# Performance work log

Hardware: AMD Instinct MI355X
Metric: run time of the kernel (lower is better)

The kernel has to match this reference:

```python
import jax, jax.numpy as jnp
import numpy as np

B = 16384; NF = 16; VOCAB = 100000; ED = 32; NNUM = 13
E = 8; T = 2; H0 = 512; H1 = 256; TH = 128
D0 = NF * ED + NNUM  # 525
EPS = 1e-5


def setup_inputs() -> dict:
    key = jax.random.key(0)
    ks = jax.random.split(key, 24)
    f32 = jnp.float32
    return {
        "categorical_x": jax.random.randint(ks[0], (B, NF), 0, VOCAB),
        "numerical_x": jax.random.normal(ks[1], (B, NNUM), f32),
        "epoch": 5,  # >= M -> MoE (not if_neuron) branch
        "emb_table": jax.random.normal(ks[2], (NF * VOCAB, ED), f32) * 0.05,
        "W0": jax.random.normal(ks[3], (E, D0, H0), f32) * 0.05,
        "b0": jnp.zeros((E, H0), f32),
        "bn0_gamma": 1.0 + 0.1 * jax.random.normal(ks[4], (H0,), f32),
        "bn0_beta": 0.1 * jax.random.normal(ks[5], (H0,), f32),
        "bn0_mean": 0.1 * jax.random.normal(ks[6], (H0,), f32),
        "bn0_var": 0.5 + jax.random.uniform(ks[7], (H0,), f32),
        "W1": jax.random.normal(ks[8], (E, H0, H1), f32) * 0.05,
        "b1": jnp.zeros((E, H1), f32),
        "bn1_gamma": 1.0 + 0.1 * jax.random.normal(ks[9], (H1,), f32),
        "bn1_beta": 0.1 * jax.random.normal(ks[10], (H1,), f32),
        "bn1_mean": 0.1 * jax.random.normal(ks[11], (H1,), f32),
        "bn1_var": 0.5 + jax.random.uniform(ks[12], (H1,), f32),
        "Wg": jax.random.normal(ks[13], (T, D0, E), f32) * 0.05,
        "bg": jnp.zeros((T, E), f32),
        "Wt1": jax.random.normal(ks[14], (T, H1, TH), f32) * 0.05,
        "bt1": jnp.zeros((T, TH), f32),
        "tbn_gamma": 1.0 + 0.1 * jax.random.normal(ks[15], (T, TH), f32),
        "tbn_beta": 0.1 * jax.random.normal(ks[16], (T, TH), f32),
        "tbn_mean": 0.1 * jax.random.normal(ks[17], (T, TH), f32),
        "tbn_var": 0.5 + jax.random.uniform(ks[18], (T, TH), f32),
        "Wt2": jax.random.normal(ks[19], (T, TH, 1), f32) * 0.05,
        "bt2": jnp.zeros((T, 1), f32),
    }


def reference(categorical_x, numerical_x, epoch, emb_table,
              W0, b0, bn0_gamma, bn0_beta, bn0_mean, bn0_var,
              W1, b1, bn1_gamma, bn1_beta, bn1_mean, bn1_var,
              Wg, bg, Wt1, bt1, tbn_gamma, tbn_beta, tbn_mean, tbn_var,
              Wt2, bt2):
    # --- embedding + concat ---
    offsets = jnp.arange(NF, dtype=categorical_x.dtype) * VOCAB
    emb = emb_table[categorical_x + offsets[None, :]].reshape(B, NF * ED)
    x = jnp.concatenate([emb, numerical_x], axis=1)  # [B, D0]

    def bn(h, g, b, m, v):  # eval-mode BatchNorm1d, params shared across experts
        return (h - m) * jax.lax.rsqrt(v + EPS) * g + b

    # --- per-expert layer 0: grouped GEMM + shared BN/ReLU (Dropout eval=id) ---
    h = jnp.einsum('bd,edk->ebk', x, W0) + b0[:, None, :]          # [E,B,H0]
    h = jax.nn.relu(bn(h, bn0_gamma, bn0_beta, bn0_mean, bn0_var))
    # --- per-expert layer 1 ---
    h = jnp.einsum('ebd,edk->ebk', h, W1) + b1[:, None, :]          # [E,B,H1]
    h = jax.nn.relu(bn(h, bn1_gamma, bn1_beta, bn1_mean, bn1_var))

    expert_output = jnp.transpose(h, (1, 0, 2))                     # [B,E,H1]
    # --- per-task softmax gates over the raw input, bmm combine ---
    gates = jax.nn.softmax(jnp.einsum('bd,tde->tbe', x, Wg) + bg[:, None, :], axis=-1)  # [T,B,E]
    fea = jnp.einsum('tbe,bek->tbk', gates, expert_output)          # [T,B,H1]

    # --- per-task tower MLP: Linear -> BN -> ReLU -> Linear, sigmoid ---
    t = jnp.einsum('tbk,tkh->tbh', fea, Wt1) + bt1[:, None, :]      # [T,B,TH]
    t = (t - tbn_mean[:, None, :]) * jax.lax.rsqrt(tbn_var[:, None, :] + EPS)
    t = jax.nn.relu(t * tbn_gamma[:, None, :] + tbn_beta[:, None, :])
    out = (jnp.einsum('tbh,tho->tbo', t, Wt2) + bt2[:, None, :])[..., 0]  # [T,B]
    return jax.nn.sigmoid(out)
```

## Files before the change

### kernel.cpp

```cpp
#include <hip/hip_runtime.h>
#include <hip/hip_bf16.h>

#define B_ 16384
#define NF_ 16
#define VOCAB_ 100000
#define ED_ 32
#define NNUM_ 13
#define E_ 8
#define T_ 2
#define H0_ 512
#define H1_ 256
#define TH_ 128
#define D0_ 525
#define K0P 640

typedef __bf16 bf16x8 __attribute__((ext_vector_type(8)));
typedef float  f32x4  __attribute__((ext_vector_type(4)));

typedef __attribute__((address_space(3))) void lds_void;
typedef __attribute__((address_space(1))) const void gbl_void;

__device__ __forceinline__ void load_lds16f(const void* g, void* l) {
  __builtin_amdgcn_global_load_lds((gbl_void*)g, (lds_void*)l, 16, 0, 0);
}

#define BARX                                        \
  do {                                              \
    asm volatile("" ::: "memory");                  \
    __builtin_amdgcn_s_barrier();                   \
    __builtin_amdgcn_sched_barrier(0);              \
    asm volatile("" ::: "memory");                  \
  } while (0)
#define LGKM0                                       \
  do {                                              \
    asm volatile("s_waitcnt lgkmcnt(0)" ::: "memory"); \
    __builtin_amdgcn_sched_barrier(0);              \
  } while (0)

__global__ __launch_bounds__(256) void k_embed(const int* __restrict__ cat,
                                               const float* __restrict__ num,
                                               const float* __restrict__ emb,
                                               __hip_bfloat16* __restrict__ x) {
  int b = blockIdx.x;
  int t = threadIdx.x;
  const int* crow = cat + b * NF_;
#pragma unroll
  for (int i = 0; i < 3; ++i) {
    int d = t + i * 256;
    if (d >= K0P) continue;
    float v;
    if (d < 512) {
      int f = d >> 5, c = d & 31;
      v = emb[((long long)(f * VOCAB_ + crow[f])) * ED_ + c];
    } else if (d < D0_) {
      v = num[b * NNUM_ + (d - 512)];
    } else {
      v = 0.f;
    }
    x[(long long)b * K0P + d] = __float2bfloat16(v);
  }
}

__global__ __launch_bounds__(256) void k_wprep(const float* __restrict__ W,
                                               __hip_bfloat16* __restrict__ Wp,
                                               int K, int N, int KP) {
  __shared__ float tile[64][65];
  int k0 = blockIdx.x * 64, n0 = blockIdx.y * 64, e = blockIdx.z;
  int tx = threadIdx.x & 63, ty = threadIdx.x >> 6;
  for (int r = ty; r < 64; r += 4) {
    int k = k0 + r;
    tile[r][tx] = (k < K) ? W[((long long)e * K + k) * N + n0 + tx] : 0.f;
  }
  __syncthreads();
  for (int r = ty; r < 64; r += 4) {
    int n = n0 + r;
    Wp[((long long)e * N + n) * KP + k0 + tx] = __float2bfloat16(tile[tx][r]);
  }
}

__global__ void k_prep_small(const float* b0, const float* g0, const float* be0,
                             const float* m0, const float* v0,
                             const float* b1, const float* g1, const float* be1,
                             const float* m1, const float* v1,
                             const float* bt1, const float* tg, const float* tb,
                             const float* tm, const float* tv,
                             float* scale0, float* ebias0, float* scale1, float* ebias1,
                             float* tscale, float* tbias) {
  int i = blockIdx.x * 256 + threadIdx.x;
  if (i < H0_) scale0[i] = g0[i] * rsqrtf(v0[i] + 1e-5f);
  if (i < H1_) scale1[i] = g1[i] * rsqrtf(v1[i] + 1e-5f);
  if (i < T_ * TH_) {
    float s = tg[i] * rsqrtf(tv[i] + 1e-5f);
    tscale[i] = s;
    tbias[i] = (bt1[i] - tm[i]) * s + tb[i];
  }
  if (i < E_ * H0_) {
    int n = i & (H0_ - 1);
    float s = g0[n] * rsqrtf(v0[n] + 1e-5f);
    ebias0[i] = (b0[i] - m0[n]) * s + be0[n];
  }
  if (i < E_ * H1_) {
    int n = i & (H1_ - 1);
    float s = g1[n] * rsqrtf(v1[n] + 1e-5f);
    ebias1[i] = (b1[i] - m1[n]) * s + be1[n];
  }
}

__global__ __launch_bounds__(256) void k_gates(const __hip_bfloat16* __restrict__ x,
                                               const float* __restrict__ Wg,
                                               const float* __restrict__ bg,
                                               float* __restrict__ gates) {
  int gidx = blockIdx.x * 256 + threadIdx.x;
  int b = gidx >> 4, te = gidx & 15;
  int t = te >> 3, e = te & 7;
  const __hip_bfloat16* xr = x + (long long)b * K0P;
  const float* wg = Wg + ((long long)t * D0_) * E_ + e;
  float acc = bg[t * E_ + e];
  int k = 0;
  for (; k + 8 <= D0_; k += 8) {
    bf16x8 xv = *reinterpret_cast<const bf16x8*>(xr + k);
#pragma unroll
    for (int j = 0; j < 8; ++j)
      acc += (float)xv[j] * wg[(long long)(k + j) * E_];
  }
  for (; k < D0_; ++k) acc += __bfloat162float(xr[k]) * wg[(long long)k * E_];
  float mx = acc;
#pragma unroll
  for (int o = 1; o < 8; o <<= 1) mx = fmaxf(mx, __shfl_xor(mx, o));
  float p = __expf(acc - mx);
  float s = p;
#pragma unroll
  for (int o = 1; o < 8; o <<= 1) s += __shfl_xor(s, o);
  gates[((long long)t * B_ + b) * E_ + e] = p / s;
}

__global__ __launch_bounds__(512, 2) void k_gemm(
    const __hip_bfloat16* __restrict__ Aall, long long strideAe, int lda,
    const __hip_bfloat16* __restrict__ Ball, long long strideBe, int ldb,
    __hip_bfloat16* __restrict__ Call, long long strideCe, int N,
    const float* __restrict__ scale, const float* __restrict__ ebias, int strideEb,
    int K) {
  __shared__ __align__(16) char As[2][2][16384];
  __shared__ __align__(16) char Bs[2][2][16384];

  const int e = blockIdx.z;
  const char* A = reinterpret_cast<const char*>(Aall + (long long)e * strideAe +
                                                (long long)blockIdx.x * 256 * lda);
  const char* Bw = reinterpret_cast<const char*>(Ball + (long long)e * strideBe +
                                                 (long long)blockIdx.y * 256 * ldb);
  const int ldab = lda * 2, ldbb = ldb * 2;

  const int tid = threadIdx.x;
  const int lane = tid & 63;
  const int wid = tid >> 6;
  const int wq_r = wid >> 2, wq_c = wid & 3;

  const int srow = tid >> 3;
  const int swz = ((tid & 7) << 4) ^ ((srow & 7) << 4);

  auto STG_A = [&](int kt, int half, int slot) {
#pragma unroll
    for (int j = 0; j < 2; ++j) {
      const int lrow = srow + j * 64;
      load_lds16f(A + (long long)(half * 128 + lrow) * ldab + kt * 128 + swz,
                  &As[slot][half][j * 8192 + tid * 16]);
    }
  };
  auto STG_B = [&](int kt, int half, int slot) {
#pragma unroll
    for (int j = 0; j < 2; ++j) {
      const int lrow = srow + j * 64;
      load_lds16f(Bw + (long long)(half * 128 + lrow) * ldbb + kt * 128 + swz,
                  &Bs[slot][half][j * 8192 + tid * 16]);
    }
  };

  bf16x8 af[2][4], bq[2][2];
  auto LDA = [&](int slot, int half) {
#pragma unroll
    for (int kk = 0; kk < 2; ++kk) {
      const int kb = kk * 64 + (lane >> 4) * 16;
#pragma unroll
      for (int m = 0; m < 4; ++m) {
        const int lrow = wq_r * 64 + m * 16 + (lane & 15);
        af[kk][m] = *reinterpret_cast<const bf16x8*>(
            &As[slot][half][lrow * 128 + (kb ^ ((lane & 7) << 4))]);
      }
    }
  };
  auto LDB = [&](int slot, int half) {
#pragma unroll
    for (int kk = 0; kk < 2; ++kk) {
      const int kb = kk * 64 + (lane >> 4) * 16;
#pragma unroll
      for (int n = 0; n < 2; ++n) {
        const int lrow = wq_c * 32 + n * 16 + (lane & 15);
        bq[kk][n] = *reinterpret_cast<const bf16x8*>(
            &Bs[slot][half][lrow * 128 + (kb ^ ((lane & 7) << 4))]);
      }
    }
  };

  f32x4 acc[2][2][4][2];
#pragma unroll
  for (int a = 0; a < 2; ++a)
#pragma unroll
    for (int b = 0; b < 2; ++b)
#pragma unroll
      for (int m = 0; m < 4; ++m)
#pragma unroll
        for (int n = 0; n < 2; ++n) acc[a][b][m][n] = (f32x4){0.f, 0.f, 0.f, 0.f};

#define MMQ(QM, QN)                                                            \
  do {                                                                         \
    __builtin_amdgcn_s_setprio(1);                                             \
    _Pragma("unroll") for (int kk = 0; kk < 2; ++kk)                           \
        _Pragma("unroll") for (int m = 0; m < 4; ++m)                          \
            _Pragma("unroll") for (int n = 0; n < 2; ++n)                      \
                acc[QM][QN][m][n] = __builtin_amdgcn_mfma_f32_16x16x32_bf16(   \
                    af[kk][m], bq[kk][n], acc[QM][QN][m][n], 0, 0, 0);         \
    __builtin_amdgcn_s_setprio(0);                                             \
  } while (0)

  const int nk = K / 64;
  const int nj = nk / 2;

  STG_A(0, 0, 0); STG_A(0, 1, 0); STG_B(0, 0, 0); STG_B(0, 1, 0);
  if (nk > 1) { STG_A(1, 0, 1); STG_B(1, 1, 1); }
  asm volatile("s_waitcnt vmcnt(4)" ::: "memory");
  BARX;

  for (int j = 0; j < nj; ++j) {
    const int t1 = 2 * j + 1, t2 = 2 * j + 2, t3 = 2 * j + 3;
    const bool more = (t2 < nk);
    LDA(0, 0); LDB(0, 0);
    STG_A(t1, 1, 1);
    BARX; LGKM0; MMQ(0, 0); BARX;
    LDB(0, 1);
    STG_B(t1, 0, 1);
    BARX; LGKM0; MMQ(0, 1); BARX;
    LDA(0, 1);
    if (more) STG_A(t2, 0, 0);
    BARX; LGKM0; MMQ(1, 1); BARX;
    LDB(0, 0);
    if (more) STG_B(t2, 1, 0);
    BARX; LGKM0; MMQ(1, 0);
    if (more) { asm volatile("s_waitcnt vmcnt(4)" ::: "memory"); }
    else      { asm volatile("s_waitcnt vmcnt(0)" ::: "memory"); }
    BARX;
    LDA(1, 0); LDB(1, 0);
    if (more) STG_A(t2, 1, 0);
    BARX; LGKM0; MMQ(0, 0); BARX;
    LDB(1, 1);
    if (more) STG_B(t2, 0, 0);
    BARX; LGKM0; MMQ(0, 1); BARX;
    LDA(1, 1);
    if (more) STG_A(t3, 0, 1);
    BARX; LGKM0; MMQ(1, 1); BARX;
    LDB(1, 0);
    if (more) STG_B(t3, 1, 1);
    BARX; LGKM0; MMQ(1, 0);
    if (more) { asm volatile("s_waitcnt vmcnt(4)" ::: "memory"); }
    BARX;
  }
#undef MMQ

  __hip_bfloat16* C = Call + (long long)e * strideCe;
  const float* eb = ebias + e * strideEb;
  const int m0 = blockIdx.x * 256, n0 = blockIdx.y * 256;
#pragma unroll
  for (int Qm = 0; Qm < 2; ++Qm)
#pragma unroll
    for (int Qn = 0; Qn < 2; ++Qn)
#pragma unroll
      for (int n = 0; n < 2; ++n) {
        const int col = n0 + Qn * 128 + wq_c * 32 + n * 16 + (lane & 15);
        const float s = scale[col];
        const float bb = eb[col];
#pragma unroll
        for (int m = 0; m < 4; ++m) {
          const int rowb = m0 + Qm * 128 + wq_r * 64 + m * 16 + (lane >> 4) * 4;
#pragma unroll
          for (int i = 0; i < 4; ++i) {
            float v = fmaxf(acc[Qm][Qn][m][n][i] * s + bb, 0.f);
            C[(long long)(rowb + i) * N + col] = __float2bfloat16(v);
          }
        }
      }
}

__global__ __launch_bounds__(256) void k_tower(
    const __hip_bfloat16* __restrict__ h1, const float* __restrict__ gates,
    const float* __restrict__ Wt1, const float* __restrict__ Wt2,
    const float* __restrict__ bt2, const float* __restrict__ tscale,
    const float* __restrict__ tbias, float* __restrict__ out) {
  __shared__ __align__(16) char Ws[TH_ * 512];
  const int tid = threadIdx.x;
  const int lane = tid & 63, wv = tid >> 6;

  const int row = blockIdx.x * 64 + wv * 16 + (lane & 15);
  const int g4 = lane >> 4;

  float gt0[8], gt1[8];
  {
    const float* gp0 = gates + (long long)row * E_;
    const float* gp1 = gates + ((long long)B_ + row) * E_;
#pragma unroll
    for (int j = 0; j < 8; ++j) { gt0[j] = gp0[j]; gt1[j] = gp1[j]; }
  }

  float fa0[8][8], fa1[8][8];
#pragma unroll
  for (int c = 0; c < 8; ++c)
#pragma unroll
    for (int j = 0; j < 8; ++j) { fa0[c][j] = 0.f; fa1[c][j] = 0.f; }

#pragma unroll
  for (int ee = 0; ee < 8; ++ee) {
    const char* hp = reinterpret_cast<const char*>(h1) +
                     (((long long)ee * B_ + row) * H1_ + g4 * 8) * 2;
    float ga = gt0[ee], gb = gt1[ee];
#pragma unroll
    for (int c = 0; c < 8; ++c) {
      bf16x8 hv = *reinterpret_cast<const bf16x8*>(hp + c * 64);
#pragma unroll
      for (int j = 0; j < 8; ++j) {
        float v = (float)hv[j];
        fa0[c][j] += ga * v;
        fa1[c][j] += gb * v;
      }
    }
  }
  bf16x8 af0[8], af1[8];
#pragma unroll
  for (int c = 0; c < 8; ++c)
#pragma unroll
    for (int j = 0; j < 8; ++j) {
      af0[c][j] = (__bf16)fa0[c][j];
      af1[c][j] = (__bf16)fa1[c][j];
    }

#pragma unroll
  for (int t = 0; t < T_; ++t) {
    if (t) __syncthreads();
    for (int it = 0; it < 16; ++it) {
      int idx = it * 256 + tid;
      int h = idx & 127, kc = idx >> 7;
      bf16x8 v;
#pragma unroll
      for (int j = 0; j < 8; ++j)
        v[j] = (__bf16)Wt1[((long long)t * H1_ + kc * 8 + j) * TH_ + h];
      int byt = h * 512 + ((kc * 16) ^ ((h & 7) << 4));
      *reinterpret_cast<bf16x8*>(Ws + byt) = v;
    }
    __syncthreads();

    f32x4 acc[8];
#pragma unroll
    for (int n = 0; n < 8; ++n) acc[n] = (f32x4){0.f, 0.f, 0.f, 0.f};
#pragma unroll
    for (int c = 0; c < 8; ++c) {
      int kb = c * 64 + g4 * 16;
#pragma unroll
      for (int n = 0; n < 8; ++n) {
        int hrow = n * 16 + (lane & 15);
        bf16x8 bv = *reinterpret_cast<const bf16x8*>(Ws + hrow * 512 + (kb ^ ((hrow & 7) << 4)));
        acc[n] = __builtin_amdgcn_mfma_f32_16x16x32_bf16(t ? af1[c] : af0[c], bv, acc[n], 0, 0, 0);
      }
    }

    float part[4] = {0.f, 0.f, 0.f, 0.f};
#pragma unroll
    for (int n = 0; n < 8; ++n) {
      int col = n * 16 + (lane & 15);
      float s = tscale[t * TH_ + col], bb = tbias[t * TH_ + col], w2 = Wt2[t * TH_ + col];
#pragma unroll
      for (int i = 0; i < 4; ++i)
        part[i] += fmaxf(acc[n][i] * s + bb, 0.f) * w2;
    }
#pragma unroll
    for (int o = 1; o < 16; o <<= 1) {
#pragma unroll
      for (int i = 0; i < 4; ++i) part[i] += __shfl_xor(part[i], o);
    }
    if ((lane & 15) == 0) {
      int rbase = blockIdx.x * 64 + wv * 16 + g4 * 4;
      float b2 = bt2[t];
#pragma unroll
      for (int i = 0; i < 4; ++i) {
        float z = part[i] + b2;
        out[(long long)t * B_ + rbase + i] = 1.f / (1.f + __expf(-z));
      }
    }
  }
}

extern "C" void kernel_launch(void* const* d_in, const int* in_sizes, int n_in,
                              void* d_out, int out_size, void* d_ws, size_t ws_size,
                              hipStream_t stream) {
  const int*   cat = (const int*)d_in[0];
  const float* num = (const float*)d_in[1];
  const float* emb = (const float*)d_in[3];
  const float* W0  = (const float*)d_in[4];
  const float* b0  = (const float*)d_in[5];
  const float* g0  = (const float*)d_in[6];
  const float* be0 = (const float*)d_in[7];
  const float* m0  = (const float*)d_in[8];
  const float* v0  = (const float*)d_in[9];
  const float* W1  = (const float*)d_in[10];
  const float* b1  = (const float*)d_in[11];
  const float* g1  = (const float*)d_in[12];
  const float* be1 = (const float*)d_in[13];
  const float* m1  = (const float*)d_in[14];
  const float* v1  = (const float*)d_in[15];
  const float* Wg  = (const float*)d_in[16];
  const float* bg  = (const float*)d_in[17];
  const float* Wt1 = (const float*)d_in[18];
  const float* bt1 = (const float*)d_in[19];
  const float* tg  = (const float*)d_in[20];
  const float* tb  = (const float*)d_in[21];
  const float* tm  = (const float*)d_in[22];
  const float* tv  = (const float*)d_in[23];
  const float* Wt2 = (const float*)d_in[24];
  const float* bt2 = (const float*)d_in[25];
  float* out = (float*)d_out;

  char* ws = (char*)d_ws;
  if (ws_size < 230719488ULL) return;

  __hip_bfloat16* x_bf = (__hip_bfloat16*)(ws + 0ULL);
  __hip_bfloat16* W0p  = (__hip_bfloat16*)(ws + 20971520ULL);
  __hip_bfloat16* W1p  = (__hip_bfloat16*)(ws + 26214400ULL);
  float* gates   = (float*)(ws + 28311552ULL);
  float* scale0  = (float*)(ws + 29360128ULL);
  float* ebias0  = (float*)(ws + 29362176ULL);
  float* scale1  = (float*)(ws + 29378560ULL);
  float* ebias1  = (float*)(ws + 29379584ULL);
  float* tscale  = (float*)(ws + 29387776ULL);
  float* tbias   = (float*)(ws + 29388800ULL);
  __hip_bfloat16* h0 = (__hip_bfloat16*)(ws + 29392896ULL);
  __hip_bfloat16* h1 = (__hip_bfloat16*)(ws + 163610624ULL);

  k_wprep<<<dim3(K0P / 64, H0_ / 64, E_), 256, 0, stream>>>(W0, W0p, D0_, H0_, K0P);
  k_wprep<<<dim3(H0_ / 64, H1_ / 64, E_), 256, 0, stream>>>(W1, W1p, H0_, H1_, H0_);
  k_prep_small<<<16, 256, 0, stream>>>(b0, g0, be0, m0, v0, b1, g1, be1, m1, v1,
                                       bt1, tg, tb, tm, tv,
                                       scale0, ebias0, scale1, ebias1, tscale, tbias);
  k_embed<<<B_, 256, 0, stream>>>(cat, num, emb, x_bf);
  k_gates<<<B_ * 16 / 256, 256, 0, stream>>>(x_bf, Wg, bg, gates);
  k_gemm<<<dim3(B_ / 256, H0_ / 256, E_), 512, 0, stream>>>(
      x_bf, 0LL, K0P, W0p, (long long)H0_ * K0P, K0P,
      h0, (long long)B_ * H0_, H0_, scale0, ebias0, H0_, K0P);
  k_gemm<<<dim3(B_ / 256, H1_ / 256, E_), 512, 0, stream>>>(
      h0, (long long)B_ * H0_, H0_, W1p, (long long)H1_ * H0_, H0_,
      h1, (long long)B_ * H1_, H1_, scale1, ebias1, H1_, H0_);
  k_tower<<<dim3(B_ / 64), 256, 0, stream>>>(h1, gates, Wt1, Wt2, bt2,
                                             tscale, tbias, out);
}
```

Before: 294.9 us.

## Split tower into separate gate-combine kernel and per-task tower GEMM kernel

The fused tower kernel, which did the gated expert combine in registers and then both task MLPs, is split in two. A new combine kernel reads h1 with coalesced 16-byte loads per thread and writes bf16 fea for both tasks to a new workspace buffer. The tower kernel then runs one task per blockIdx.y. This is meant to cut register pressure (the old kernel held 128 float accumulators) and to add parallelism. In exchange it adds an extra 16 MB round trip through memory and one more launch, and it needs a larger workspace.

Measured after the change: 257.6 us. 1.14x faster.

```diff
diff --git a/kernel.cpp b/kernel.cpp
--- a/kernel.cpp
+++ b/kernel.cpp
@@ -289,108 +289,108 @@
       }
 }
 
-__global__ __launch_bounds__(256) void k_tower(
-    const __hip_bfloat16* __restrict__ h1, const float* __restrict__ gates,
-    const float* __restrict__ Wt1, const float* __restrict__ Wt2,
-    const float* __restrict__ bt2, const float* __restrict__ tscale,
-    const float* __restrict__ tbias, float* __restrict__ out) {
+__global__ __launch_bounds__(256) void k_combine(const __hip_bfloat16* __restrict__ h1,
+                                                 const float* __restrict__ gates,
+                                                 __hip_bfloat16* __restrict__ fea) {
+  const int idx = blockIdx.x * 256 + threadIdx.x;
+  const int b = idx >> 5, c = idx & 31;
+  const f32x4* gp0 = reinterpret_cast<const f32x4*>(gates + (long long)b * E_);
+  const f32x4* gp1 = reinterpret_cast<const f32x4*>(gates + ((long long)B_ + b) * E_);
+  const f32x4 g0lo = gp0[0], g0hi = gp0[1];
+  const f32x4 g1lo = gp1[0], g1hi = gp1[1];
+
+  float a0[8], a1[8];
+#pragma unroll
+  for (int j = 0; j < 8; ++j) { a0[j] = 0.f; a1[j] = 0.f; }
+
+#pragma unroll
+  for (int ee = 0; ee < 8; ++ee) {
+    bf16x8 hv = *reinterpret_cast<const bf16x8*>(
+        h1 + ((long long)ee * B_ + b) * H1_ + c * 8);
+    const float ga = (ee < 4) ? g0lo[ee & 3] : g0hi[ee & 3];
+    const float gb = (ee < 4) ? g1lo[ee & 3] : g1hi[ee & 3];
+#pragma unroll
+    for (int j = 0; j < 8; ++j) {
+      float v = (float)hv[j];
+      a0[j] += ga * v;
+      a1[j] += gb * v;
+    }
+  }
+  bf16x8 o0, o1;
+#pragma unroll
+  for (int j = 0; j < 8; ++j) { o0[j] = (__bf16)a0[j]; o1[j] = (__bf16)a1[j]; }
+  *reinterpret_cast<bf16x8*>(fea + (long long)b * H1_ + c * 8) = o0;
+  *reinterpret_cast<bf16x8*>(fea + ((long long)B_ + b) * H1_ + c * 8) = o1;
+}
+
+__global__ __launch_bounds__(256) void k_tower2(
+    const __hip_bfloat16* __restrict__ fea, const float* __restrict__ Wt1,
+    const float* __restrict__ Wt2, const float* __restrict__ bt2,
+    const float* __restrict__ tscale, const float* __restrict__ tbias,
+    float* __restrict__ out) {
   __shared__ __align__(16) char Ws[TH_ * 512];
+  const int t = blockIdx.y;
   const int tid = threadIdx.x;
   const int lane = tid & 63, wv = tid >> 6;
 
   const int row = blockIdx.x * 64 + wv * 16 + (lane & 15);
   const int g4 = lane >> 4;
 
-  float gt0[8], gt1[8];
+  for (int it = 0; it < 16; ++it) {
+    int idx = it * 256 + tid;
+    int h = idx & 127, kc = idx >> 7;
+    bf16x8 v;
+#pragma unroll
+    for (int j = 0; j < 8; ++j)
+      v[j] = (__bf16)Wt1[((long long)t * H1_ + kc * 8 + j) * TH_ + h];
+    int byt = h * 512 + ((kc * 16) ^ ((h & 7) << 4));
+    *reinterpret_cast<bf16x8*>(Ws + byt) = v;
+  }
+
+  bf16x8 af[8];
   {
-    const float* gp0 = gates + (long long)row * E_;
-    const float* gp1 = gates + ((long long)B_ + row) * E_;
-#pragma unroll
-    for (int j = 0; j < 8; ++j) { gt0[j] = gp0[j]; gt1[j] = gp1[j]; }
-  }
-
-  float fa0[8][8], fa1[8][8];
-#pragma unroll
-  for (int c = 0; c < 8; ++c)
-#pragma unroll
-    for (int j = 0; j < 8; ++j) { fa0[c][j] = 0.f; fa1[c][j] = 0.f; }
-
-#pragma unroll
-  for (int ee = 0; ee < 8; ++ee) {
-    const char* hp = reinterpret_cast<const char*>(h1) +
-                     (((long long)ee * B_ + row) * H1_ + g4 * 8) * 2;
-    float ga = gt0[ee], gb = gt1[ee];
-#pragma unroll
-    for (int c = 0; c < 8; ++c) {
-      bf16x8 hv = *reinterpret_cast<const bf16x8*>(hp + c * 64);
-#pragma unroll
-      for (int j = 0; j < 8; ++j) {
-        float v = (float)hv[j];
-        fa0[c][j] += ga * v;
-        fa1[c][j] += gb * v;
-      }
-    }
-  }
-  bf16x8 af0[8], af1[8];
-#pragma unroll
-  for (int c = 0; c < 8; ++c)
-#pragma unroll
-    for (int j = 0; j < 8; ++j) {
-      af0[c][j] = (__bf16)fa0[c][j];
-      af1[c][j] = (__bf16)fa1[c][j];
-    }
-
-#pragma unroll
-  for (int t = 0; t < T_; ++t) {
-    if (t) __syncthreads();
-    for (int it = 0; it < 16; ++it) {
-      int idx = it * 256 + tid;
-      int h = idx & 127, kc = idx >> 7;
-      bf16x8 v;
-#pragma unroll
-      for (int j = 0; j < 8; ++j)
-        v[j] = (__bf16)Wt1[((long long)t * H1_ + kc * 8 + j) * TH_ + h];
-      int byt = h * 512 + ((kc * 16) ^ ((h & 7) << 4));
-      *reinterpret_cast<bf16x8*>(Ws + byt) = v;
-    }
-    __syncthreads();
-
-    f32x4 acc[8];
-#pragma unroll
-    for (int n = 0; n < 8; ++n) acc[n] = (f32x4){0.f, 0.f, 0.f, 0.f};
-#pragma unroll
-    for (int c = 0; c < 8; ++c) {
-      int kb = c * 64 + g4 * 16;
-#pragma unroll
-      for (int n = 0; n < 8; ++n) {
-        int hrow = n * 16 + (lane & 15);
-        bf16x8 bv = *reinterpret_cast<const bf16x8*>(Ws + hrow * 512 + (kb ^ ((hrow & 7) << 4)));
-        acc[n] = __builtin_amdgcn_mfma_f32_16x16x32_bf16(t ? af1[c] : af0[c], bv, acc[n], 0, 0, 0);
-      }
-    }
-
-    float part[4] = {0.f, 0.f, 0.f, 0.f};
+    const __hip_bfloat16* fp = fea + ((long long)t * B_ + row) * H1_ + g4 * 8;
+#pragma unroll
+    for (int c = 0; c < 8; ++c)
+      af[c] = *reinterpret_cast<const bf16x8*>(fp + c * 32);
+  }
+  __syncthreads();
+
+  f32x4 acc[8];
+#pragma unroll
+  for (int n = 0; n < 8; ++n) acc[n] = (f32x4){0.f, 0.f, 0.f, 0.f};
+#pragma unroll
+  for (int c = 0; c < 8; ++c) {
+    int kb = c * 64 + g4 * 16;
 #pragma unroll
     for (int n = 0; n < 8; ++n) {
-      int col = n * 16 + (lane & 15);
-      float s = tscale[t * TH_ + col], bb = tbias[t * TH_ + col], w2 = Wt2[t * TH_ + col];
-#pragma unroll
-      for (int i = 0; i < 4; ++i)
-        part[i] += fmaxf(acc[n][i] * s + bb, 0.f) * w2;
-    }
-#pragma unroll
-    for (int o = 1; o < 16; o <<= 1) {
-#pragma unroll
-      for (int i = 0; i < 4; ++i) part[i] += __shfl_xor(part[i], o);
-    }
-    if ((lane & 15) == 0) {
-      int rbase = blockIdx.x * 64 + wv * 16 + g4 * 4;
-      float b2 = bt2[t];
-#pragma unroll
-      for (int i = 0; i < 4; ++i) {
-        float z = part[i] + b2;
-        out[(long long)t * B_ + rbase + i] = 1.f / (1.f + __expf(-z));
-      }
+      int hrow = n * 16 + (lane & 15);
+      bf16x8 bv = *reinterpret_cast<const bf16x8*>(Ws + hrow * 512 + (kb ^ ((hrow & 7) << 4)));
+      acc[n] = __builtin_amdgcn_mfma_f32_16x16x32_bf16(af[c], bv, acc[n], 0, 0, 0);
+    }
+  }
+
+  float part[4] = {0.f, 0.f, 0.f, 0.f};
+#pragma unroll
+  for (int n = 0; n < 8; ++n) {
+    int col = n * 16 + (lane & 15);
+    float s = tscale[t * TH_ + col], bb = tbias[t * TH_ + col], w2 = Wt2[t * TH_ + col];
+#pragma unroll
+    for (int i = 0; i < 4; ++i)
+      part[i] += fmaxf(acc[n][i] * s + bb, 0.f) * w2;
+  }
+#pragma unroll
+  for (int o = 1; o < 16; o <<= 1) {
+#pragma unroll
+    for (int i = 0; i < 4; ++i) part[i] += __shfl_xor(part[i], o);
+  }
+  if ((lane & 15) == 0) {
+    int rbase = blockIdx.x * 64 + wv * 16 + g4 * 4;
+    float b2 = bt2[t];
+#pragma unroll
+    for (int i = 0; i < 4; ++i) {
+      float z = part[i] + b2;
+      out[(long long)t * B_ + rbase + i] = 1.f / (1.f + __expf(-z));
     }
   }
 }
@@ -426,7 +426,7 @@
   float* out = (float*)d_out;
 
   char* ws = (char*)d_ws;
-  if (ws_size < 230719488ULL) return;
+  if (ws_size < 247496704ULL) return;
 
   __hip_bfloat16* x_bf = (__hip_bfloat16*)(ws + 0ULL);
   __hip_bfloat16* W0p  = (__hip_bfloat16*)(ws + 20971520ULL);
@@ -438,8 +438,9 @@
   float* ebias1  = (float*)(ws + 29379584ULL);
   float* tscale  = (float*)(ws + 29387776ULL);
   float* tbias   = (float*)(ws + 29388800ULL);
-  __hip_bfloat16* h0 = (__hip_bfloat16*)(ws + 29392896ULL);
-  __hip_bfloat16* h1 = (__hip_bfloat16*)(ws + 163610624ULL);
+  __hip_bfloat16* h0  = (__hip_bfloat16*)(ws + 29392896ULL);
+  __hip_bfloat16* h1  = (__hip_bfloat16*)(ws + 163610624ULL);
+  __hip_bfloat16* fea = (__hip_bfloat16*)(ws + 230719488ULL);
 
   k_wprep<<<dim3(K0P / 64, H0_ / 64, E_), 256, 0, stream>>>(W0, W0p, D0_, H0_, K0P);
   k_wprep<<<dim3(H0_ / 64, H1_ / 64, E_), 256, 0, stream>>>(W1, W1p, H0_, H1_, H0_);
@@ -454,6 +455,7 @@
   k_gemm<<<dim3(B_ / 256, H1_ / 256, E_), 512, 0, stream>>>(
       h0, (long long)B_ * H0_, H0_, W1p, (long long)H1_ * H0_, H0_,
       h1, (long long)B_ * H1_, H1_, scale1, ebias1, H1_, H0_);
-  k_tower<<<dim3(B_ / 64), 256, 0, stream>>>(h1, gates, Wt1, Wt2, bt2,
-                                             tscale, tbias, out);
-}
+  k_combine<<<B_ * H1_ / 8 / 256, 256, 0, stream>>>(h1, gates, fea);
+  k_tower2<<<dim3(B_ / 64, T_), 256, 0, stream>>>(fea, Wt1, Wt2, bt2,
+                                                  tscale, tbias, out);
+}
```
